# Kernel tuning notes

Hardware: AMD Instinct MI355X
Metric: run time of the kernel (lower is better)

Reference implementation:

```python
import jax, jax.numpy as jnp
import numpy as np

EPS = 1e-5  # torch F.layer_norm default

def _layer_norm(x):
    mu = jnp.mean(x, axis=-1, keepdims=True)
    var = jnp.mean((x - mu) ** 2, axis=-1, keepdims=True)
    return (x - mu) * jax.lax.rsqrt(var + EPS)

def setup_inputs() -> dict:
    key = jax.random.key(0)
    k1, k2, k3, k4 = jax.random.split(key, 4)
    B, T, d, n = 4, 32, 256, 1024
    return {
        "x_seq": jax.random.normal(k1, (B, T, d), jnp.float32),
        "targets": jax.random.normal(k2, (B, T, d), jnp.float32),
        "E": jax.random.normal(k3, (d, n), jnp.float32) * 0.1,
        "Dy": jax.random.normal(k4, (n, d), jnp.float32) * 0.1,
    }

def reference(x_seq, targets, E, Dy):
    B, T, d = x_seq.shape
    n = E.shape[1]
    # Precompute per-step neuron activations (no cross-step dependency here)
    x_neurons = jax.nn.relu(_layer_norm(x_seq @ E))      # [B,T,n]
    tgt_neurons = jax.nn.relu(_layer_norm(targets @ E))  # [B,T,n]
    # update at step t uses targets[:, t+1]; last step does no update
    tgt_next = jnp.concatenate(
        [tgt_neurons[:, 1:], jnp.zeros_like(tgt_neurons[:, :1])], axis=1)
    upd_mask = jnp.arange(T) < (T - 1)  # [T]

    G0 = jnp.tile(0.01 * jnp.eye(n, dtype=x_seq.dtype)[None], (B, 1, 1))

    def step(G, inp):
        xn, tn, m = inp  # [B,n], [B,n], scalar bool
        p1 = jnp.einsum('bn,bnm->bm', xn, G)
        p2 = jnp.einsum('bn,bnm->bm', p1, G)
        p3 = jnp.einsum('bn,bnm->bm', p2, G)
        reasoning = jnp.maximum(p1, jnp.maximum(p2, p3))
        y = jax.nn.relu(reasoning @ Dy)  # [B,d]
        # rank-1 Hebbian max-update: G = max(G, 0.5 * xn tn^T)
        upd = 0.5 * xn[:, :, None] * tn[:, None, :]
        G_new = jnp.where(m, jnp.maximum(G, upd), G)
        return G_new, y

    xs = (jnp.swapaxes(x_neurons, 0, 1),  # [T,B,n]
          jnp.swapaxes(tgt_next, 0, 1),   # [T,B,n]
          upd_mask)                       # [T]
    _, ys = jax.lax.scan(step, G0, xs)    # ys: [T,B,d]
    return jnp.swapaxes(ys, 0, 1)         # [B,T,d]
```

## Files before the change

kernel.cpp:

```cpp
#include <hip/hip_runtime.h>

#define BB 4
#define TT 32
#define DD 256
#define NN 1024

#define XN_OFF   0
#define TN_OFF   131072
#define PB_OFF   262144
#define RB_OFF   524288
#define FLG_OFF  655360
#define FLG_WORDS 6144
#define WS_END   (FLG_OFF + FLG_WORDS)

__global__ __launch_bounds__(256) void precompute_kernel(
    const float* __restrict__ x_seq, const float* __restrict__ targets,
    const float* __restrict__ E, float* __restrict__ ws)
{
    __shared__ float xr[4][DD];
    __shared__ float redS[4][4], redSS[4][4];
    const int blk = blockIdx.x;
    const int bt0 = blk * 2, bt1 = bt0 + 1;
    const int tid = threadIdx.x;
    const int lane = tid & 63, w = tid >> 6;

    xr[0][tid] = x_seq[(size_t)bt0 * DD + tid];
    xr[1][tid] = x_seq[(size_t)bt1 * DD + tid];
    xr[2][tid] = targets[(size_t)bt0 * DD + tid];
    xr[3][tid] = targets[(size_t)bt1 * DD + tid];
    __syncthreads();

    const float4* E4 = (const float4*)E;
    float4 acc[4];
#pragma unroll
    for (int r = 0; r < 4; ++r) acc[r] = make_float4(0.f, 0.f, 0.f, 0.f);
#pragma unroll 4
    for (int k = 0; k < DD; ++k) {
        float4 e = E4[(size_t)k * (NN / 4) + tid];
#pragma unroll
        for (int r = 0; r < 4; ++r) {
            float xv = xr[r][k];
            acc[r].x += xv * e.x; acc[r].y += xv * e.y;
            acc[r].z += xv * e.z; acc[r].w += xv * e.w;
        }
    }
    float s[4], ss[4];
#pragma unroll
    for (int r = 0; r < 4; ++r) {
        s[r]  = acc[r].x + acc[r].y + acc[r].z + acc[r].w;
        ss[r] = acc[r].x*acc[r].x + acc[r].y*acc[r].y + acc[r].z*acc[r].z + acc[r].w*acc[r].w;
    }
#pragma unroll
    for (int d = 1; d < 64; d <<= 1) {
#pragma unroll
        for (int r = 0; r < 4; ++r) {
            s[r]  += __shfl_xor(s[r], d, 64);
            ss[r] += __shfl_xor(ss[r], d, 64);
        }
    }
    if (lane == 0) {
#pragma unroll
        for (int r = 0; r < 4; ++r) { redS[w][r] = s[r]; redSS[w][r] = ss[r]; }
    }
    __syncthreads();
#pragma unroll
    for (int r = 0; r < 4; ++r) {
        s[r]  = redS[0][r] + redS[1][r] + redS[2][r] + redS[3][r];
        ss[r] = redSS[0][r] + redSS[1][r] + redSS[2][r] + redSS[3][r];
    }
#pragma unroll
    for (int r = 0; r < 4; ++r) {
        const float mu  = s[r] * (1.0f / NN);
        const float var = ss[r] * (1.0f / NN) - mu * mu;
        const float inv = rsqrtf(var + 1e-5f);
        float4 o;
        o.x = fmaxf(0.f, (acc[r].x - mu) * inv);
        o.y = fmaxf(0.f, (acc[r].y - mu) * inv);
        o.z = fmaxf(0.f, (acc[r].z - mu) * inv);
        o.w = fmaxf(0.f, (acc[r].w - mu) * inv);
        const int bt = (r & 1) ? bt1 : bt0;
        float* dst = nullptr;
        if (r < 2) dst = ws + XN_OFF + (size_t)bt * NN;
        else if ((bt & 31) > 0) dst = ws + TN_OFF + (size_t)(bt - 1) * NN;
        if (dst) ((float4*)dst)[tid] = o;
    }
}

__device__ __forceinline__ float ald(const float* p) {
    return __hip_atomic_load(p, __ATOMIC_RELAXED, __HIP_MEMORY_SCOPE_AGENT);
}
__device__ __forceinline__ unsigned long long ald64(const unsigned long long* p) {
    return __hip_atomic_load(p, __ATOMIC_RELAXED, __HIP_MEMORY_SCOPE_AGENT);
}
__device__ __forceinline__ void ast(float* p, float v) {
    __hip_atomic_store(p, v, __ATOMIC_RELAXED, __HIP_MEMORY_SCOPE_AGENT);
}
__device__ __forceinline__ unsigned aldu_rlx(const unsigned* p) {
    return __hip_atomic_load(p, __ATOMIC_RELAXED, __HIP_MEMORY_SCOPE_AGENT);
}

__global__ __launch_bounds__(512, 1) void mega_kernel(
    const float* __restrict__ Dy, float* __restrict__ out, float* __restrict__ ws)
{
    __shared__ float sh[6144];
    const int blk = blockIdx.x;
    const int tid = threadIdx.x;

    float* pb     = ws + PB_OFF;
    float* rb     = ws + RB_OFF;
    unsigned* flg = (unsigned*)(ws + FLG_OFF);

    if (blk < 192) {
        const int stage = blk >> 6;
        const int b     = (blk >> 4) & 3;
        const int wg    = blk & 15;
        const int lane  = tid & 63;
        const int w     = tid >> 6;
        const int colbase = wg * 64 + w * 8;
        const int row0    = lane * 16;
        const float* xn = ws + XN_OFF + (size_t)b * TT * NN;
        const float* tn = ws + TN_OFF + (size_t)b * TT * NN;
        unsigned* myflag = flg + ((size_t)(stage * 4 + b) * 16 + wg) * 32;
        const unsigned* inflags =
            (stage > 0) ? flg + ((size_t)((stage - 1) * 4 + b) * 16) * 32 : (const unsigned*)0;
        unsigned seen = 0;

        float G[16][8];
#pragma unroll
        for (int i = 0; i < 16; ++i)
#pragma unroll
            for (int c = 0; c < 8; ++c)
                G[i][c] = (row0 + i == colbase + c) ? 0.01f : 0.0f;

#pragma unroll 1
        for (int t = 0; t < TT; t += 4) {
            const int bt = b * TT + t;
            float* pbase = pb + (size_t)bt * 2 * NN;

            float v1own[4] = {0.f, 0.f, 0.f, 0.f};

            if (stage != 0) {
                const unsigned tgt = (unsigned)(t + 4);
                if (tid < 64) {
                    if (seen < tgt) {
                        const unsigned* p = inflags + (size_t)(tid & 15) * 32;
                        int g = 0;
                        for (;;) {
                            unsigned v = aldu_rlx(p);
                            if (v > seen) seen = v;
                            if (__all(seen >= tgt)) break;
                            __builtin_amdgcn_s_sleep(1);
                            if (++g > (1 << 22)) break;
                        }
                    }
                }
                __syncthreads();
                asm volatile("" ::: "memory");
                if (stage == 2) {
#pragma unroll
                    for (int j = 0; j < 4; ++j)
                        v1own[j] = ald(pbase + (size_t)(2 * j) * NN + colbase + (lane & 7));
                }
                union { unsigned long long u; float f[2]; } cv[4];
#pragma unroll
                for (int j = 0; j < 4; ++j) {
                    const float* src = pbase + (size_t)(2 * j) * NN + ((stage == 1) ? 0 : NN);
                    cv[j].u = ald64((const unsigned long long*)src + tid);
                }
                const int e0 = 2 * tid;
#pragma unroll
                for (int j = 0; j < 4; ++j) {
                    sh[j * 1152 + e0 + (e0 >> 4)]     = cv[j].f[0];
                    sh[j * 1152 + e0 + 1 + (e0 >> 4)] = cv[j].f[1];
                }
                __syncthreads();
            }

            float xsave[16];
#pragma unroll
            for (int j = 0; j < 4; ++j) {
                const int tj = t + j;
                float in[16];
                if (stage == 0) {
                    const float4* xp = (const float4*)(xn + (size_t)tj * NN + row0);
                    float4 q0 = xp[0], q1 = xp[1], q2 = xp[2], q3 = xp[3];
                    in[0]=q0.x; in[1]=q0.y; in[2]=q0.z; in[3]=q0.w;
                    in[4]=q1.x; in[5]=q1.y; in[6]=q1.z; in[7]=q1.w;
                    in[8]=q2.x; in[9]=q2.y; in[10]=q2.z; in[11]=q2.w;
                    in[12]=q3.x; in[13]=q3.y; in[14]=q3.z; in[15]=q3.w;
                    if (j == 3) {
#pragma unroll
                        for (int k = 0; k < 16; ++k) xsave[k] = in[k];
                    }
                } else {
#pragma unroll
                    for (int k = 0; k < 16; ++k) in[k] = sh[j * 1152 + lane * 17 + k];
                }

                float acc[8] = {0.f,0.f,0.f,0.f,0.f,0.f,0.f,0.f};
#pragma unroll
                for (int i = 0; i < 16; ++i)
#pragma unroll
                    for (int c = 0; c < 8; ++c) acc[c] += in[i] * G[i][c];

                float t4[8];
#pragma unroll
                for (int c = 0; c < 8; ++c) t4[c] = __shfl_xor(acc[c], 4, 64);
                const bool k2 = (lane & 4) != 0;
                float s4[4];
#pragma unroll
                for (int k = 0; k < 4; ++k) s4[k] = k2 ? (acc[4+k] + t4[4+k]) : (acc[k] + t4[k]);
                float t2[4];
#pragma unroll
                for (int k = 0; k < 4; ++k) t2[k] = __shfl_xor(s4[k], 2, 64);
                const bool k1 = (lane & 2) != 0;
                float s2[2];
#pragma unroll
                for (int k = 0; k < 2; ++k) s2[k] = k1 ? (s4[2+k] + t2[2+k]) : (s4[k] + t2[k]);
                float t1[2];
#pragma unroll
                for (int k = 0; k < 2; ++k) t1[k] = __shfl_xor(s2[k], 1, 64);
                float v = (lane & 1) ? (s2[1] + t1[1]) : (s2[0] + t1[0]);
                v += __shfl_xor(v, 8, 64);
                v += __shfl_xor(v, 16, 64);
                v += __shfl_xor(v, 32, 64);

                if (stage == 0) {
                    if (lane < 8) ast(pbase + (size_t)(2 * j) * NN + colbase + lane, v);
                } else if (stage == 1) {
                    if (lane < 8) ast(pbase + (size_t)(2 * j) * NN + NN + colbase + lane, v);
                } else {
                    const int c = colbase + (lane & 7);
                    const float v2own = sh[j * 1152 + c + (c >> 4)];
                    float r = fmaxf(v, fmaxf(v1own[j], v2own));
                    if (lane < 8) ast(rb + (size_t)(bt + j) * NN + colbase + lane, r);
                }

                if (j < 3) {
                    float x[16];
                    if (stage == 0) {
#pragma unroll
                        for (int k = 0; k < 16; ++k) x[k] = in[k];
                    } else {
                        const float4* xp = (const float4*)(xn + (size_t)tj * NN + row0);
                        float4 q0 = xp[0], q1 = xp[1], q2 = xp[2], q3 = xp[3];
                        x[0]=q0.x; x[1]=q0.y; x[2]=q0.z; x[3]=q0.w;
                        x[4]=q1.x; x[5]=q1.y; x[6]=q1.z; x[7]=q1.w;
                        x[8]=q2.x; x[9]=q2.y; x[10]=q2.z; x[11]=q2.w;
                        x[12]=q3.x; x[13]=q3.y; x[14]=q3.z; x[15]=q3.w;
                    }
                    const float4 ta = *(const float4*)(tn + (size_t)tj * NN + colbase);
                    const float4 tb = *(const float4*)(tn + (size_t)tj * NN + colbase + 4);
                    const float tv[8] = {0.5f*ta.x, 0.5f*ta.y, 0.5f*ta.z, 0.5f*ta.w,
                                         0.5f*tb.x, 0.5f*tb.y, 0.5f*tb.z, 0.5f*tb.w};
#pragma unroll
                    for (int c = 0; c < 8; ++c)
#pragma unroll
                        for (int i = 0; i < 16; ++i)
                            G[i][c] = fmaxf(G[i][c], x[i] * tv[c]);
                }
            }

            __syncthreads();
            if (tid == 0)
                __hip_atomic_store(myflag, (unsigned)(t + 4),
                                   __ATOMIC_RELEASE, __HIP_MEMORY_SCOPE_AGENT);

            if (t + 3 < TT - 1) {
                const int tj = t + 3;
                float x[16];
                if (stage == 0) {
#pragma unroll
                    for (int k = 0; k < 16; ++k) x[k] = xsave[k];
                } else {
                    const float4* xp = (const float4*)(xn + (size_t)tj * NN + row0);
                    float4 q0 = xp[0], q1 = xp[1], q2 = xp[2], q3 = xp[3];
                    x[0]=q0.x; x[1]=q0.y; x[2]=q0.z; x[3]=q0.w;
                    x[4]=q1.x; x[5]=q1.y; x[6]=q1.z; x[7]=q1.w;
                    x[8]=q2.x; x[9]=q2.y; x[10]=q2.z; x[11]=q2.w;
                    x[12]=q3.x; x[13]=q3.y; x[14]=q3.z; x[15]=q3.w;
                }
                const float4 ta = *(const float4*)(tn + (size_t)tj * NN + colbase);
                const float4 tb = *(const float4*)(tn + (size_t)tj * NN + colbase + 4);
                const float tv[8] = {0.5f*ta.x, 0.5f*ta.y, 0.5f*ta.z, 0.5f*ta.w,
                                     0.5f*tb.x, 0.5f*tb.y, 0.5f*tb.z, 0.5f*tb.w};
#pragma unroll
                for (int c = 0; c < 8; ++c)
#pragma unroll
                    for (int i = 0; i < 16; ++i)
                        G[i][c] = fmaxf(G[i][c], x[i] * tv[c]);
            }
        }
    } else {
        const int k   = blk - 192;
        const int b   = k >> 3;
        const int t0  = (k & 7) * 4;
        const int bt0 = b * TT + t0;
        if (tid < 64) {
            const unsigned* p = flg + ((size_t)(2 * 4 + b) * 16 + (tid & 15)) * 32;
            const unsigned tgt = (unsigned)(t0 + 4);
            int g = 0;
            for (;;) {
                unsigned v = aldu_rlx(p);
                if (__all(v >= tgt)) break;
                __builtin_amdgcn_s_sleep(1);
                if (++g > (1 << 22)) break;
            }
        }
        __syncthreads();
        asm volatile("" ::: "memory");
#pragma unroll
        for (int j = 0; j < 4; ++j) {
            const float* r = rb + (size_t)(bt0 + j) * NN;
            sh[tid * 4 + j]         = ald(r + tid);
            sh[(tid + 512) * 4 + j] = ald(r + tid + 512);
        }
        __syncthreads();
        const int d = tid & 255, h = tid >> 8;
        float acc[4] = {0.f, 0.f, 0.f, 0.f};
        const int n0 = h * 512;
#pragma unroll 8
        for (int n = n0; n < n0 + 512; ++n) {
            const float dv = Dy[(size_t)n * DD + d];
            const float4 rv = *(const float4*)&sh[n * 4];
            acc[0] += rv.x * dv; acc[1] += rv.y * dv;
            acc[2] += rv.z * dv; acc[3] += rv.w * dv;
        }
#pragma unroll
        for (int j = 0; j < 4; ++j) sh[4096 + (h * 4 + j) * 256 + d] = acc[j];
        __syncthreads();
        if (tid < 256) {
#pragma unroll
            for (int j = 0; j < 4; ++j)
                out[(size_t)(bt0 + j) * DD + tid] =
                    fmaxf(0.f, sh[4096 + j * 256 + tid] + sh[4096 + (4 + j) * 256 + tid]);
        }
    }
}

extern "C" void kernel_launch(void* const* d_in, const int* in_sizes, int n_in,
                              void* d_out, int out_size, void* d_ws, size_t ws_size,
                              hipStream_t stream) {
    const float* x_seq   = (const float*)d_in[0];
    const float* targets = (const float*)d_in[1];
    const float* E       = (const float*)d_in[2];
    const float* Dy      = (const float*)d_in[3];
    float* out = (float*)d_out;
    float* ws  = (float*)d_ws;

    hipMemsetAsync(ws + FLG_OFF, 0, (size_t)FLG_WORDS * sizeof(unsigned), stream);

    precompute_kernel<<<BB * TT / 2, 256, 0, stream>>>(x_seq, targets, E, ws);
    mega_kernel<<<224, 512, 0, stream>>>(Dy, out, ws);
}
```

Measured before the change: 247.4 us.

## Stride row mapping, prefetch next step inputs directly, skip zero-target G updates

Changes the row-to-lane mapping from contiguous 16-row chunks to a 64-stride interleave, so each step's input vector can be read coalesced straight from global memory. This removes the LDS staging buffer and its extra syncthreads. The next time step's input is double-buffered into registers while the current matvec runs. Hebbian max-updates are skipped for columns whose target activation is exactly zero (common after ReLU), tested with a wave-uniform readfirstlane. The cost is more scalar global loads and branches in place of vectorized float4 loads.

```diff
diff --git a/kernel.cpp b/kernel.cpp
--- a/kernel.cpp
+++ b/kernel.cpp
@@ -89,9 +89,6 @@
 __device__ __forceinline__ float ald(const float* p) {
     return __hip_atomic_load(p, __ATOMIC_RELAXED, __HIP_MEMORY_SCOPE_AGENT);
 }
-__device__ __forceinline__ unsigned long long ald64(const unsigned long long* p) {
-    return __hip_atomic_load(p, __ATOMIC_RELAXED, __HIP_MEMORY_SCOPE_AGENT);
-}
 __device__ __forceinline__ void ast(float* p, float v) {
     __hip_atomic_store(p, v, __ATOMIC_RELAXED, __HIP_MEMORY_SCOPE_AGENT);
 }
@@ -117,7 +114,6 @@
         const int lane  = tid & 63;
         const int w     = tid >> 6;
         const int colbase = wg * 64 + w * 8;
-        const int row0    = lane * 16;
         const float* xn = ws + XN_OFF + (size_t)b * TT * NN;
         const float* tn = ws + TN_OFF + (size_t)b * TT * NN;
         unsigned* myflag = flg + ((size_t)(stage * 4 + b) * 16 + wg) * 32;
@@ -130,14 +126,15 @@
         for (int i = 0; i < 16; ++i)
 #pragma unroll
             for (int c = 0; c < 8; ++c)
-                G[i][c] = (row0 + i == colbase + c) ? 0.01f : 0.0f;
+                G[i][c] = (i * 64 + lane == colbase + c) ? 0.01f : 0.0f;
 
 #pragma unroll 1
         for (int t = 0; t < TT; t += 4) {
             const int bt = b * TT + t;
             float* pbase = pb + (size_t)bt * 2 * NN;
 
-            float v1own[4] = {0.f, 0.f, 0.f, 0.f};
+            float v1a = 0.f, v1b = 0.f, v1c = 0.f, v1d = 0.f;
+            float v2a = 0.f, v2b = 0.f, v2c = 0.f, v2d = 0.f;
 
             if (stage != 0) {
                 const unsigned tgt = (unsigned)(t + 4);
@@ -157,51 +154,50 @@
                 __syncthreads();
                 asm volatile("" ::: "memory");
                 if (stage == 2) {
-#pragma unroll
-                    for (int j = 0; j < 4; ++j)
-                        v1own[j] = ald(pbase + (size_t)(2 * j) * NN + colbase + (lane & 7));
-                }
-                union { unsigned long long u; float f[2]; } cv[4];
-#pragma unroll
-                for (int j = 0; j < 4; ++j) {
-                    const float* src = pbase + (size_t)(2 * j) * NN + ((stage == 1) ? 0 : NN);
-                    cv[j].u = ald64((const unsigned long long*)src + tid);
-                }
-                const int e0 = 2 * tid;
-#pragma unroll
-                for (int j = 0; j < 4; ++j) {
-                    sh[j * 1152 + e0 + (e0 >> 4)]     = cv[j].f[0];
-                    sh[j * 1152 + e0 + 1 + (e0 >> 4)] = cv[j].f[1];
-                }
-                __syncthreads();
-            }
-
-            float xsave[16];
+                    const int co8 = colbase + (lane & 7);
+                    v1a = ald(pbase + (size_t)0 * NN + co8);
+                    v1b = ald(pbase + (size_t)2 * NN + co8);
+                    v1c = ald(pbase + (size_t)4 * NN + co8);
+                    v1d = ald(pbase + (size_t)6 * NN + co8);
+                    v2a = ald(pbase + (size_t)0 * NN + NN + co8);
+                    v2b = ald(pbase + (size_t)2 * NN + NN + co8);
+                    v2c = ald(pbase + (size_t)4 * NN + NN + co8);
+                    v2d = ald(pbase + (size_t)6 * NN + NN + co8);
+                }
+            }
+
+            const size_t soff = (stage == 1) ? 0 : (size_t)NN;
+            float inA[16], inB[16];
+            if (stage == 0) {
+#pragma unroll
+                for (int i = 0; i < 16; ++i) inA[i] = xn[(size_t)t * NN + i * 64 + lane];
+            } else {
+#pragma unroll
+                for (int i = 0; i < 16; ++i) inA[i] = ald(pbase + soff + i * 64 + lane);
+            }
+
 #pragma unroll
             for (int j = 0; j < 4; ++j) {
                 const int tj = t + j;
-                float in[16];
-                if (stage == 0) {
-                    const float4* xp = (const float4*)(xn + (size_t)tj * NN + row0);
-                    float4 q0 = xp[0], q1 = xp[1], q2 = xp[2], q3 = xp[3];
-                    in[0]=q0.x; in[1]=q0.y; in[2]=q0.z; in[3]=q0.w;
-                    in[4]=q1.x; in[5]=q1.y; in[6]=q1.z; in[7]=q1.w;
-                    in[8]=q2.x; in[9]=q2.y; in[10]=q2.z; in[11]=q2.w;
-                    in[12]=q3.x; in[13]=q3.y; in[14]=q3.z; in[15]=q3.w;
-                    if (j == 3) {
-#pragma unroll
-                        for (int k = 0; k < 16; ++k) xsave[k] = in[k];
-                    }
-                } else {
-#pragma unroll
-                    for (int k = 0; k < 16; ++k) in[k] = sh[j * 1152 + lane * 17 + k];
+                const float (&inC)[16] = (j & 1) ? inB : inA;
+                float (&inN)[16]       = (j & 1) ? inA : inB;
+                if (j < 3) {
+                    if (stage == 0) {
+#pragma unroll
+                        for (int i = 0; i < 16; ++i)
+                            inN[i] = xn[(size_t)(tj + 1) * NN + i * 64 + lane];
+                    } else {
+#pragma unroll
+                        for (int i = 0; i < 16; ++i)
+                            inN[i] = ald(pbase + (size_t)(2 * (j + 1)) * NN + soff + i * 64 + lane);
+                    }
                 }
 
                 float acc[8] = {0.f,0.f,0.f,0.f,0.f,0.f,0.f,0.f};
 #pragma unroll
                 for (int i = 0; i < 16; ++i)
 #pragma unroll
-                    for (int c = 0; c < 8; ++c) acc[c] += in[i] * G[i][c];
+                    for (int c = 0; c < 8; ++c) acc[c] += inC[i] * G[i][c];
 
                 float t4[8];
 #pragma unroll
@@ -230,9 +226,9 @@
                 } else if (stage == 1) {
                     if (lane < 8) ast(pbase + (size_t)(2 * j) * NN + NN + colbase + lane, v);
                 } else {
-                    const int c = colbase + (lane & 7);
-                    const float v2own = sh[j * 1152 + c + (c >> 4)];
-                    float r = fmaxf(v, fmaxf(v1own[j], v2own));
+                    const float v1o = (j == 0) ? v1a : (j == 1) ? v1b : (j == 2) ? v1c : v1d;
+                    const float v2o = (j == 0) ? v2a : (j == 1) ? v2b : (j == 2) ? v2c : v2d;
+                    float r = fmaxf(v, fmaxf(v1o, v2o));
                     if (lane < 8) ast(rb + (size_t)(bt + j) * NN + colbase + lane, r);
                 }
 
@@ -240,24 +236,23 @@
                     float x[16];
                     if (stage == 0) {
 #pragma unroll
-                        for (int k = 0; k < 16; ++k) x[k] = in[k];
+                        for (int k = 0; k < 16; ++k) x[k] = inC[k];
                     } else {
-                        const float4* xp = (const float4*)(xn + (size_t)tj * NN + row0);
-                        float4 q0 = xp[0], q1 = xp[1], q2 = xp[2], q3 = xp[3];
-                        x[0]=q0.x; x[1]=q0.y; x[2]=q0.z; x[3]=q0.w;
-                        x[4]=q1.x; x[5]=q1.y; x[6]=q1.z; x[7]=q1.w;
-                        x[8]=q2.x; x[9]=q2.y; x[10]=q2.z; x[11]=q2.w;
-                        x[12]=q3.x; x[13]=q3.y; x[14]=q3.z; x[15]=q3.w;
+#pragma unroll
+                        for (int k = 0; k < 16; ++k) x[k] = xn[(size_t)tj * NN + k * 64 + lane];
                     }
                     const float4 ta = *(const float4*)(tn + (size_t)tj * NN + colbase);
                     const float4 tb = *(const float4*)(tn + (size_t)tj * NN + colbase + 4);
                     const float tv[8] = {0.5f*ta.x, 0.5f*ta.y, 0.5f*ta.z, 0.5f*ta.w,
                                          0.5f*tb.x, 0.5f*tb.y, 0.5f*tb.z, 0.5f*tb.w};
 #pragma unroll
-                    for (int c = 0; c < 8; ++c)
-#pragma unroll
-                        for (int i = 0; i < 16; ++i)
-                            G[i][c] = fmaxf(G[i][c], x[i] * tv[c]);
+                    for (int c = 0; c < 8; ++c) {
+                        if (__builtin_amdgcn_readfirstlane(__float_as_uint(tv[c])) != 0u) {
+#pragma unroll
+                            for (int i = 0; i < 16; ++i)
+                                G[i][c] = fmaxf(G[i][c], x[i] * tv[c]);
+                        }
+                    }
                 }
             }
 
@@ -271,24 +266,23 @@
                 float x[16];
                 if (stage == 0) {
 #pragma unroll
-                    for (int k = 0; k < 16; ++k) x[k] = xsave[k];
+                    for (int k = 0; k < 16; ++k) x[k] = inB[k];
                 } else {
-                    const float4* xp = (const float4*)(xn + (size_t)tj * NN + row0);
-                    float4 q0 = xp[0], q1 = xp[1], q2 = xp[2], q3 = xp[3];
-                    x[0]=q0.x; x[1]=q0.y; x[2]=q0.z; x[3]=q0.w;
-                    x[4]=q1.x; x[5]=q1.y; x[6]=q1.z; x[7]=q1.w;
-                    x[8]=q2.x; x[9]=q2.y; x[10]=q2.z; x[11]=q2.w;
-                    x[12]=q3.x; x[13]=q3.y; x[14]=q3.z; x[15]=q3.w;
+#pragma unroll
+                    for (int k = 0; k < 16; ++k) x[k] = xn[(size_t)tj * NN + k * 64 + lane];
                 }
                 const float4 ta = *(const float4*)(tn + (size_t)tj * NN + colbase);
                 const float4 tb = *(const float4*)(tn + (size_t)tj * NN + colbase + 4);
                 const float tv[8] = {0.5f*ta.x, 0.5f*ta.y, 0.5f*ta.z, 0.5f*ta.w,
                                      0.5f*tb.x, 0.5f*tb.y, 0.5f*tb.z, 0.5f*tb.w};
 #pragma unroll
-                for (int c = 0; c < 8; ++c)
-#pragma unroll
-                    for (int i = 0; i < 16; ++i)
-                        G[i][c] = fmaxf(G[i][c], x[i] * tv[c]);
+                for (int c = 0; c < 8; ++c) {
+                    if (__builtin_amdgcn_readfirstlane(__float_as_uint(tv[c])) != 0u) {
+#pragma unroll
+                        for (int i = 0; i < 16; ++i)
+                            G[i][c] = fmaxf(G[i][c], x[i] * tv[c]);
+                    }
+                }
             }
         }
     } else {
```

Measured after the change: 200.4 us (median of 2 runs). 19.0% less time.
